# Kernel optimization log

Measured on AMD Instinct MI355X. Metric: run time of the kernel, lower is better.

The kernel has to match this reference:

```python
import jax, jax.numpy as jnp
import numpy as np

B, A, C, H, W = 4, 5, 64, 128, 128


def _base_grid(h, w):
    # torch F.affine_grid with align_corners=False: pixel-center normalized coords
    xs = (2.0 * jnp.arange(w, dtype=jnp.float32) + 1.0) / w - 1.0
    ys = (2.0 * jnp.arange(h, dtype=jnp.float32) + 1.0) / h - 1.0
    X, Y = jnp.meshgrid(xs, ys)  # [h,w]
    return jnp.stack([X, Y, jnp.ones_like(X)], axis=-1)  # [h,w,3]


def _grid_sample(img, grid):
    # img [C,H,W]; grid [H,W,2] = (x,y) normalized; bilinear, zeros padding, align_corners=False
    c, h, w = img.shape
    ix = ((grid[..., 0] + 1.0) * w - 1.0) * 0.5
    iy = ((grid[..., 1] + 1.0) * h - 1.0) * 0.5
    ix0 = jnp.floor(ix); iy0 = jnp.floor(iy)
    ix1 = ix0 + 1.0; iy1 = iy0 + 1.0
    wx1 = ix - ix0; wy1 = iy - iy0
    wx0 = 1.0 - wx1; wy0 = 1.0 - wy1

    def gather(iyf, ixf):
        valid = (iyf >= 0) & (iyf <= h - 1) & (ixf >= 0) & (ixf <= w - 1)
        iyc = jnp.clip(iyf.astype(jnp.int32), 0, h - 1)
        ixc = jnp.clip(ixf.astype(jnp.int32), 0, w - 1)
        return img[:, iyc, ixc] * valid[None].astype(img.dtype)  # [C,H,W]

    return (gather(iy0, ix0) * (wy0 * wx0)[None]
            + gather(iy0, ix1) * (wy0 * wx1)[None]
            + gather(iy1, ix0) * (wy1 * wx0)[None]
            + gather(iy1, ix1) * (wy1 * wx1)[None])


_sample_batch = jax.vmap(_grid_sample)


def setup_inputs() -> dict:
    key = jax.random.key(0)
    k1, k2, k3 = jax.random.split(key, 3)
    feats = jax.random.normal(k1, (B, A, C, H, W), dtype=jnp.float32)
    trans_matrices = jax.random.normal(k2, (B, A, A, 4, 4), dtype=jnp.float32)
    num_agent_tensor = jax.random.randint(k3, (B, A), 1, A + 1, dtype=jnp.int64)
    return {"feats": feats, "trans_matrices": trans_matrices,
            "num_agent_tensor": num_agent_tensor}


def reference(feats, trans_matrices, num_agent_tensor):
    b, a, c, h, w = feats.shape
    T = trans_matrices  # [B,A(target i),A(neighbor j),4,4]
    zeros = jnp.zeros(T.shape[:3], T.dtype)
    ones = jnp.ones_like(zeros)
    # theta_rot = [[T00, T01, 0], [T10, T11, 0]]
    theta_rot = jnp.stack([
        jnp.stack([T[..., 0, 0], T[..., 0, 1], zeros], axis=-1),
        jnp.stack([T[..., 1, 0], T[..., 1, 1], zeros], axis=-1)], axis=-2)
    x_t = 4.0 * T[..., 0, 3] / 128.0
    y_t = -(4.0 * T[..., 1, 3]) / 128.0
    theta_trans = jnp.stack([
        jnp.stack([ones, zeros, x_t], axis=-1),
        jnp.stack([zeros, ones, y_t], axis=-1)], axis=-2)
    base = _base_grid(h, w)  # [H,W,3]
    grid_rot = jnp.einsum('hwk,bijrk->bijhwr', base, theta_rot)
    grid_trans = jnp.einsum('hwk,bijrk->bijhwr', base, theta_trans)
    n = b * a * a
    # neighbor feature feats[b, j] broadcast over target index i
    feats_nb = jnp.broadcast_to(feats[:, None], (b, a, a, c, h, w)).reshape(n, c, h, w)
    w1 = _sample_batch(feats_nb, grid_rot.reshape(n, h, w, 2))
    w2 = _sample_batch(w1, grid_trans.reshape(n, h, w, 2)).reshape(b, a, a, c, h, w)
    na = num_agent_tensor[:, 0]  # [B]
    ar = jnp.arange(a)
    valid = ((ar[None, :, None] < na[:, None, None])
             & (ar[None, None, :] < na[:, None, None])
             & (ar[:, None] != ar[None, :])[None])  # [B,A_i,A_j]
    fused = feats + jnp.sum(w2 * valid[..., None, None, None].astype(feats.dtype), axis=2)
    # agents2batch: concatenate per-agent slices along batch dim -> [A*B, C, H, W]
    return fused.transpose(1, 0, 2, 3, 4).reshape(a * b, c, h, w)
```

## Files before the change

### kernel.cpp

```cpp
#include <hip/hip_runtime.h>


constexpr int Bc = 4, Ac = 5, Cc = 64, Hc = 128, Wc = 128;
constexpr int HWc = Hc * Wc;
constexpr int NP  = Bc * Ac;
constexpr int NG  = Cc / 4;
constexpr int TW = 64, TH = 4;
constexpr int WW = TW + 1, WH = TH + 1, WSZ = WW * WH;
constexpr size_t WS_NEED = (size_t)NP * Cc * HWc * sizeof(float);

__global__ __launch_bounds__(256)
void fafmimo_repack(const float* __restrict__ feats, float4* __restrict__ ws)
{
    const int idx  = (int)(blockIdx.x * 256 + threadIdx.x);
    const int pix4 = (idx & 4095) * 4;
    const int t    = idx >> 12;
    const int g    = t & 15;
    const int p    = t >> 4;
    const float* s = feats + ((size_t)p * Cc + g * 4) * HWc + pix4;
    const float4 r0 = *(const float4*)(s);
    const float4 r1 = *(const float4*)(s + HWc);
    const float4 r2 = *(const float4*)(s + 2 * HWc);
    const float4 r3 = *(const float4*)(s + 3 * HWc);
    float4* d = ws + ((size_t)p * NG + g) * HWc + pix4;
    d[0] = make_float4(r0.x, r1.x, r2.x, r3.x);
    d[1] = make_float4(r0.y, r1.y, r2.y, r3.y);
    d[2] = make_float4(r0.z, r1.z, r2.z, r3.z);
    d[3] = make_float4(r0.w, r1.w, r2.w, r3.w);
}

__global__ __launch_bounds__(256)
void fafmimo_main(const float4* __restrict__ ws,
                  const float* __restrict__ trans,
                  const int*   __restrict__ num_agent,
                  float*       __restrict__ out)
{
    __shared__ float4 w1s[WSZ];

    const int z  = (int)blockIdx.z;
    const int bi = z % NP;
    const int g  = z / NP;
    const int b  = bi / Ac;
    const int i  = bi - b * Ac;
    const int tx = (int)threadIdx.x, ty = (int)threadIdx.y;
    const int tid = ty * TW + tx;
    const int x0 = (int)blockIdx.x * TW, y0 = (int)blockIdx.y * TH;
    const int x  = x0 + tx, y = y0 + ty;
    const int pix = y * Wc + x;
    const int na = num_agent[b * Ac];

    const float xv  = (2.0f * (float)x  + 1.0f) / 128.0f - 1.0f;
    const float yv  = (2.0f * (float)y  + 1.0f) / 128.0f - 1.0f;
    const float xv0 = (2.0f * (float)x0 + 1.0f) / 128.0f - 1.0f;
    const float yv0 = (2.0f * (float)y0 + 1.0f) / 128.0f - 1.0f;

    float4 acc = ws[((size_t)bi * NG + g) * HWc + pix];

    if (i < na) {
        for (int j = 0; j < Ac; ++j) {
            if (j == i || j >= na) continue;

            const float* Tm = trans + (size_t)((b * Ac + i) * Ac + j) * 16;
            const float r00 = Tm[0], r01 = Tm[1], t03 = Tm[3];
            const float r10 = Tm[4], r11 = Tm[5], t13 = Tm[7];
            const float x_t =  (4.0f * t03) / 128.0f;
            const float y_t = -(4.0f * t13) / 128.0f;

            const int fdx = (int)floorf(((xv0 + x_t + 1.0f) * 128.0f - 1.0f) * 0.5f) - x0;
            const int fdy = (int)floorf(((yv0 + y_t + 1.0f) * 128.0f - 1.0f) * 0.5f) - y0;

            const float4* __restrict__ pj =
                ws + ((size_t)((b * Ac + j) * NG) + g) * HWc;

            for (int e = tid; e < WSZ; e += TW * TH) {
                const int ry = e / WW, rx = e - ry * WW;
                const int jy = y0 + fdy + ry, jx = x0 + fdx + rx;
                const int jyc = min(max(jy, 0), 127);
                const int jxc = min(max(jx, 0), 127);

                const float Xs = (2.0f * (float)jxc + 1.0f) / 128.0f - 1.0f;
                const float Ys = (2.0f * (float)jyc + 1.0f) / 128.0f - 1.0f;
                const float gx = Xs * r00 + Ys * r01;
                const float gy = Xs * r10 + Ys * r11;
                const float ixs = ((gx + 1.0f) * 128.0f - 1.0f) * 0.5f;
                const float iys = ((gy + 1.0f) * 128.0f - 1.0f) * 0.5f;
                const float sx0 = floorf(ixs), sy0 = floorf(iys);
                const float u1 = ixs - sx0, v1 = iys - sy0;
                const float u0 = 1.0f - u1, v0 = 1.0f - v1;

                const bool xin = (sx0 >= 0.0f) & (sx0 <= 126.0f);
                const float a  = xin ? u0 : ((sx0 == -1.0f)  ? u1 : 0.0f);
                const float bb = xin ? u1 : ((sx0 == 127.0f) ? u0 : 0.0f);
                const int xb = min(max((int)sx0, 0), 126);

                const bool vr0 = (sy0 >= 0.0f) & (sy0 <= 127.0f);
                const bool vr1 = (sy0 >= -1.0f) & (sy0 <= 126.0f);
                const float wr0 = v0 * (vr0 ? 1.0f : 0.0f);
                const float wr1 = v1 * (vr1 ? 1.0f : 0.0f);
                const int o0 = min(max((int)sy0, 0), 127) * Wc + xb;
                const int o1 = min(max((int)sy0 + 1, 0), 127) * Wc + xb;

                const float4 t0a = pj[o0], t0b = pj[o0 + 1];
                const float4 t1a = pj[o1], t1b = pj[o1 + 1];
                float4 w1;
                w1.x = wr0 * fmaf(a, t0a.x, bb * t0b.x) + wr1 * fmaf(a, t1a.x, bb * t1b.x);
                w1.y = wr0 * fmaf(a, t0a.y, bb * t0b.y) + wr1 * fmaf(a, t1a.y, bb * t1b.y);
                w1.z = wr0 * fmaf(a, t0a.z, bb * t0b.z) + wr1 * fmaf(a, t1a.z, bb * t1b.z);
                w1.w = wr0 * fmaf(a, t0a.w, bb * t0b.w) + wr1 * fmaf(a, t1a.w, bb * t1b.w);
                w1s[e] = w1;
            }
            __syncthreads();

            const float ix2 = ((xv + x_t + 1.0f) * 128.0f - 1.0f) * 0.5f;
            const float iy2 = ((yv + y_t + 1.0f) * 128.0f - 1.0f) * 0.5f;
            const int jx0 = x + fdx, jy0 = y + fdy;
            const float fx1 = ix2 - (float)jx0, fx0 = 1.0f - fx1;
            const float fy1 = iy2 - (float)jy0, fy0 = 1.0f - fy1;
            const float vx0 = (jx0 >= 0 && jx0 <= 127) ? 1.0f : 0.0f;
            const float vx1 = (jx0 >= -1 && jx0 <= 126) ? 1.0f : 0.0f;
            const float vy0 = (jy0 >= 0 && jy0 <= 127) ? 1.0f : 0.0f;
            const float vy1 = (jy0 >= -1 && jy0 <= 126) ? 1.0f : 0.0f;
            const float w00 = fy0 * vy0 * fx0 * vx0;
            const float w01 = fy0 * vy0 * fx1 * vx1;
            const float w10 = fy1 * vy1 * fx0 * vx0;
            const float w11 = fy1 * vy1 * fx1 * vx1;

            const int base = ty * WW + tx;
            const float4 s00 = w1s[base],      s01 = w1s[base + 1];
            const float4 s10 = w1s[base + WW], s11 = w1s[base + WW + 1];
            acc.x += w00 * s00.x + w01 * s01.x + w10 * s10.x + w11 * s11.x;
            acc.y += w00 * s00.y + w01 * s01.y + w10 * s10.y + w11 * s11.y;
            acc.z += w00 * s00.z + w01 * s01.z + w10 * s10.z + w11 * s11.z;
            acc.w += w00 * s00.w + w01 * s01.w + w10 * s10.w + w11 * s11.w;
            __syncthreads();
        }
    }

    float* __restrict__ ob =
        out + ((size_t)(i * Bc + b) * Cc + g * 4) * HWc + pix;
    __builtin_nontemporal_store(acc.x, ob);
    __builtin_nontemporal_store(acc.y, ob + HWc);
    __builtin_nontemporal_store(acc.z, ob + 2 * HWc);
    __builtin_nontemporal_store(acc.w, ob + 3 * HWc);
}

constexpr int CHK = 16;
__global__ __launch_bounds__(256)
void fafmimo_direct(const float* __restrict__ feats,
                    const float* __restrict__ trans,
                    const int*   __restrict__ num_agent,
                    float*       __restrict__ out)
{
    const int z  = (int)blockIdx.z;
    const int bi = z % NP;
    const int c0 = (z / NP) * CHK;
    const int b  = bi / Ac;
    const int i  = bi - b * Ac;
    const int x  = (int)(blockIdx.x * 64 + threadIdx.x);
    const int y  = (int)(blockIdx.y * 4  + threadIdx.y);
    const int pix = y * Wc + x;
    const int na = num_agent[b * Ac];

    const float xv = (2.0f * (float)x + 1.0f) / 128.0f - 1.0f;
    const float yv = (2.0f * (float)y + 1.0f) / 128.0f - 1.0f;

    const float* __restrict__ fi =
        feats + (size_t)(b * Ac + i) * Cc * HWc + (size_t)c0 * HWc;
    float* __restrict__ ob =
        out + (size_t)(i * Bc + b) * Cc * HWc + (size_t)c0 * HWc;

    float acc[CHK];
    #pragma unroll
    for (int k = 0; k < CHK; ++k) acc[k] = fi[k * HWc + pix];

    if (i < na) {
        for (int j = 0; j < Ac; ++j) {
            if (j == i || j >= na) continue;
            const float* Tm = trans + (size_t)((b * Ac + i) * Ac + j) * 16;
            const float r00 = Tm[0], r01 = Tm[1], t03 = Tm[3];
            const float r10 = Tm[4], r11 = Tm[5], t13 = Tm[7];
            const float x_t =  (4.0f * t03) / 128.0f;
            const float y_t = -(4.0f * t13) / 128.0f;
            const float ix2 = ((xv + x_t + 1.0f) * 128.0f - 1.0f) * 0.5f;
            const float iy2 = ((yv + y_t + 1.0f) * 128.0f - 1.0f) * 0.5f;
            const float fx0 = floorf(ix2), fy0 = floorf(iy2);
            const float wx1 = ix2 - fx0,   wy1 = iy2 - fy0;
            const float wx0 = 1.0f - wx1,  wy0 = 1.0f - wy1;

            int off[8]; float wA[8], wB[8];
            #pragma unroll
            for (int cy = 0; cy < 2; ++cy) {
                #pragma unroll
                for (int cx = 0; cx < 2; ++cx) {
                    const float jyf = fy0 + (float)cy;
                    const float jxf = fx0 + (float)cx;
                    const bool v2 = (jyf >= 0.0f) & (jyf <= 127.0f)
                                  & (jxf >= 0.0f) & (jxf <= 127.0f);
                    const float w2 = (cy ? wy1 : wy0) * (cx ? wx1 : wx0)
                                   * (v2 ? 1.0f : 0.0f);
                    const int jy = min(max((int)jyf, 0), 127);
                    const int jx = min(max((int)jxf, 0), 127);
                    const float Xs = (2.0f * (float)jx + 1.0f) / 128.0f - 1.0f;
                    const float Ys = (2.0f * (float)jy + 1.0f) / 128.0f - 1.0f;
                    const float gx = Xs * r00 + Ys * r01;
                    const float gy = Xs * r10 + Ys * r11;
                    const float ixs = ((gx + 1.0f) * 128.0f - 1.0f) * 0.5f;
                    const float iys = ((gy + 1.0f) * 128.0f - 1.0f) * 0.5f;
                    const float sx0 = floorf(ixs), sy0 = floorf(iys);
                    const float u1 = ixs - sx0, v1 = iys - sy0;
                    const float u0 = 1.0f - u1,  v0f = 1.0f - v1;
                    const bool xin = (sx0 >= 0.0f) & (sx0 <= 126.0f);
                    const float a  = xin ? u0 : ((sx0 == -1.0f)  ? u1 : 0.0f);
                    const float bbp = xin ? u1 : ((sx0 == 127.0f) ? u0 : 0.0f);
                    const int xb = min(max((int)sx0, 0), 126);
                    const int e = (cy * 2 + cx) * 2;
                    #pragma unroll
                    for (int r = 0; r < 2; ++r) {
                        const float syr = sy0 + (float)r;
                        const bool vy = (syr >= 0.0f) & (syr <= 127.0f);
                        const float wyr = (r ? v1 : v0f) * (vy ? 1.0f : 0.0f) * w2;
                        const int syc = min(max((int)syr, 0), 127);
                        off[e + r] = syc * Wc + xb;
                        wA[e + r]  = wyr * a;
                        wB[e + r]  = wyr * bbp;
                    }
                }
            }

            const float* __restrict__ fj =
                feats + (size_t)(b * Ac + j) * Cc * HWc + (size_t)c0 * HWc;
            #pragma unroll 4
            for (int k = 0; k < CHK; ++k) {
                const float* __restrict__ p = fj + (size_t)k * HWc;
                float s0 = 0.0f, s1 = 0.0f;
                #pragma unroll
                for (int r = 0; r < 8; ++r) {
                    s0 = fmaf(wA[r], p[off[r]],     s0);
                    s1 = fmaf(wB[r], p[off[r] + 1], s1);
                }
                acc[k] += s0 + s1;
            }
        }
    }

    #pragma unroll
    for (int k = 0; k < CHK; ++k)
        __builtin_nontemporal_store(acc[k], &ob[k * HWc + pix]);
}

extern "C" void kernel_launch(void* const* d_in, const int* in_sizes, int n_in,
                              void* d_out, int out_size, void* d_ws, size_t ws_size,
                              hipStream_t stream) {
    const float* feats     = (const float*)d_in[0];
    const float* trans     = (const float*)d_in[1];
    const int*   num_agent = (const int*)d_in[2];
    float* out = (float*)d_out;

    if (ws_size >= WS_NEED) {
        float4* ws = (float4*)d_ws;
        hipLaunchKernelGGL(fafmimo_repack, dim3(NP * NG * (HWc / 4) / 256),
                           dim3(256), 0, stream, feats, ws);
        dim3 grid(Wc / TW, Hc / TH, NP * NG);
        dim3 block(TW, TH, 1);
        hipLaunchKernelGGL(fafmimo_main, grid, block, 0, stream,
                           ws, trans, num_agent, out);
    } else {
        dim3 grid(Wc / 64, Hc / 4, NP * 4);
        dim3 block(64, 4, 1);
        hipLaunchKernelGGL(fafmimo_direct, grid, block, 0, stream,
                           feats, trans, num_agent, out);
    }
}
```

Measured before the change: 211.1 us.

## Process four channel groups per block to amortize first-stage coordinate math

Each block of the main kernel now handles four float4 channel groups instead of one. The rotation-sample coordinates, weights and clamped offsets are computed once per window element and reused across the four groups. The second-stage weights are likewise reused, and the grid shrinks by a factor of four. The repack kernel also switches to nontemporal vector loads. The cost is four times the shared memory per block, more registers for four accumulators, and fewer blocks in flight.

```diff
diff --git a/kernel.cpp b/kernel.cpp
--- a/kernel.cpp
+++ b/kernel.cpp
@@ -1,12 +1,15 @@
 #include <hip/hip_runtime.h>
 
+
+typedef float floatv4 __attribute__((ext_vector_type(4)));
 
 constexpr int Bc = 4, Ac = 5, Cc = 64, Hc = 128, Wc = 128;
 constexpr int HWc = Hc * Wc;
 constexpr int NP  = Bc * Ac;
 constexpr int NG  = Cc / 4;
+constexpr int GPB = 4;
 constexpr int TW = 64, TH = 4;
-constexpr int WW = TW + 1, WH = TH + 1, WSZ = WW * WH;
+constexpr int WW = TW + 1, WSZ = WW * (TH + 1);
 constexpr size_t WS_NEED = (size_t)NP * Cc * HWc * sizeof(float);
 
 __global__ __launch_bounds__(256)
@@ -17,11 +20,12 @@
     const int t    = idx >> 12;
     const int g    = t & 15;
     const int p    = t >> 4;
-    const float* s = feats + ((size_t)p * Cc + g * 4) * HWc + pix4;
-    const float4 r0 = *(const float4*)(s);
-    const float4 r1 = *(const float4*)(s + HWc);
-    const float4 r2 = *(const float4*)(s + 2 * HWc);
-    const float4 r3 = *(const float4*)(s + 3 * HWc);
+    const floatv4* s =
+        (const floatv4*)(feats + ((size_t)p * Cc + g * 4) * HWc + pix4);
+    const floatv4 r0 = __builtin_nontemporal_load(s);
+    const floatv4 r1 = __builtin_nontemporal_load(s + HWc / 4);
+    const floatv4 r2 = __builtin_nontemporal_load(s + 2 * (HWc / 4));
+    const floatv4 r3 = __builtin_nontemporal_load(s + 3 * (HWc / 4));
     float4* d = ws + ((size_t)p * NG + g) * HWc + pix4;
     d[0] = make_float4(r0.x, r1.x, r2.x, r3.x);
     d[1] = make_float4(r0.y, r1.y, r2.y, r3.y);
@@ -35,11 +39,12 @@
                   const int*   __restrict__ num_agent,
                   float*       __restrict__ out)
 {
-    __shared__ float4 w1s[WSZ];
+    __shared__ float4 w1s[GPB][WSZ];
 
     const int z  = (int)blockIdx.z;
     const int bi = z % NP;
-    const int g  = z / NP;
+    const int q  = z / NP;
+    const int g0 = q * GPB;
     const int b  = bi / Ac;
     const int i  = bi - b * Ac;
     const int tx = (int)threadIdx.x, ty = (int)threadIdx.y;
@@ -54,7 +59,10 @@
     const float xv0 = (2.0f * (float)x0 + 1.0f) / 128.0f - 1.0f;
     const float yv0 = (2.0f * (float)y0 + 1.0f) / 128.0f - 1.0f;
 
-    float4 acc = ws[((size_t)bi * NG + g) * HWc + pix];
+    float4 acc[GPB];
+    #pragma unroll
+    for (int cg = 0; cg < GPB; ++cg)
+        acc[cg] = ws[((size_t)bi * NG + g0 + cg) * HWc + pix];
 
     if (i < na) {
         for (int j = 0; j < Ac; ++j) {
@@ -69,8 +77,10 @@
             const int fdx = (int)floorf(((xv0 + x_t + 1.0f) * 128.0f - 1.0f) * 0.5f) - x0;
             const int fdy = (int)floorf(((yv0 + y_t + 1.0f) * 128.0f - 1.0f) * 0.5f) - y0;
 
-            const float4* __restrict__ pj =
-                ws + ((size_t)((b * Ac + j) * NG) + g) * HWc;
+            const float4* __restrict__ pj0 = ws + ((size_t)((b * Ac + j) * NG) + g0) * HWc;
+            const float4* __restrict__ pj1 = pj0 + HWc;
+            const float4* __restrict__ pj2 = pj0 + 2 * HWc;
+            const float4* __restrict__ pj3 = pj0 + 3 * HWc;
 
             for (int e = tid; e < WSZ; e += TW * TH) {
                 const int ry = e / WW, rx = e - ry * WW;
@@ -100,14 +110,19 @@
                 const int o0 = min(max((int)sy0, 0), 127) * Wc + xb;
                 const int o1 = min(max((int)sy0 + 1, 0), 127) * Wc + xb;
 
-                const float4 t0a = pj[o0], t0b = pj[o0 + 1];
-                const float4 t1a = pj[o1], t1b = pj[o1 + 1];
-                float4 w1;
-                w1.x = wr0 * fmaf(a, t0a.x, bb * t0b.x) + wr1 * fmaf(a, t1a.x, bb * t1b.x);
-                w1.y = wr0 * fmaf(a, t0a.y, bb * t0b.y) + wr1 * fmaf(a, t1a.y, bb * t1b.y);
-                w1.z = wr0 * fmaf(a, t0a.z, bb * t0b.z) + wr1 * fmaf(a, t1a.z, bb * t1b.z);
-                w1.w = wr0 * fmaf(a, t0a.w, bb * t0b.w) + wr1 * fmaf(a, t1a.w, bb * t1b.w);
-                w1s[e] = w1;
+                #pragma unroll
+                for (int cg = 0; cg < GPB; ++cg) {
+                    const float4* __restrict__ pg =
+                        (cg == 0) ? pj0 : (cg == 1) ? pj1 : (cg == 2) ? pj2 : pj3;
+                    const float4 t0a = pg[o0], t0b = pg[o0 + 1];
+                    const float4 t1a = pg[o1], t1b = pg[o1 + 1];
+                    float4 w1;
+                    w1.x = wr0 * fmaf(a, t0a.x, bb * t0b.x) + wr1 * fmaf(a, t1a.x, bb * t1b.x);
+                    w1.y = wr0 * fmaf(a, t0a.y, bb * t0b.y) + wr1 * fmaf(a, t1a.y, bb * t1b.y);
+                    w1.z = wr0 * fmaf(a, t0a.z, bb * t0b.z) + wr1 * fmaf(a, t1a.z, bb * t1b.z);
+                    w1.w = wr0 * fmaf(a, t0a.w, bb * t0b.w) + wr1 * fmaf(a, t1a.w, bb * t1b.w);
+                    w1s[cg][e] = w1;
+                }
             }
             __syncthreads();
 
@@ -126,22 +141,28 @@
             const float w11 = fy1 * vy1 * fx1 * vx1;
 
             const int base = ty * WW + tx;
-            const float4 s00 = w1s[base],      s01 = w1s[base + 1];
-            const float4 s10 = w1s[base + WW], s11 = w1s[base + WW + 1];
-            acc.x += w00 * s00.x + w01 * s01.x + w10 * s10.x + w11 * s11.x;
-            acc.y += w00 * s00.y + w01 * s01.y + w10 * s10.y + w11 * s11.y;
-            acc.z += w00 * s00.z + w01 * s01.z + w10 * s10.z + w11 * s11.z;
-            acc.w += w00 * s00.w + w01 * s01.w + w10 * s10.w + w11 * s11.w;
+            #pragma unroll
+            for (int cg = 0; cg < GPB; ++cg) {
+                const float4 s00 = w1s[cg][base],      s01 = w1s[cg][base + 1];
+                const float4 s10 = w1s[cg][base + WW], s11 = w1s[cg][base + WW + 1];
+                acc[cg].x += w00 * s00.x + w01 * s01.x + w10 * s10.x + w11 * s11.x;
+                acc[cg].y += w00 * s00.y + w01 * s01.y + w10 * s10.y + w11 * s11.y;
+                acc[cg].z += w00 * s00.z + w01 * s01.z + w10 * s10.z + w11 * s11.z;
+                acc[cg].w += w00 * s00.w + w01 * s01.w + w10 * s10.w + w11 * s11.w;
+            }
             __syncthreads();
         }
     }
 
-    float* __restrict__ ob =
-        out + ((size_t)(i * Bc + b) * Cc + g * 4) * HWc + pix;
-    __builtin_nontemporal_store(acc.x, ob);
-    __builtin_nontemporal_store(acc.y, ob + HWc);
-    __builtin_nontemporal_store(acc.z, ob + 2 * HWc);
-    __builtin_nontemporal_store(acc.w, ob + 3 * HWc);
+    #pragma unroll
+    for (int cg = 0; cg < GPB; ++cg) {
+        float* __restrict__ ob =
+            out + ((size_t)(i * Bc + b) * Cc + (g0 + cg) * 4) * HWc + pix;
+        __builtin_nontemporal_store(acc[cg].x, ob);
+        __builtin_nontemporal_store(acc[cg].y, ob + HWc);
+        __builtin_nontemporal_store(acc[cg].z, ob + 2 * HWc);
+        __builtin_nontemporal_store(acc[cg].w, ob + 3 * HWc);
+    }
 }
 
 constexpr int CHK = 16;
@@ -260,7 +281,7 @@
         float4* ws = (float4*)d_ws;
         hipLaunchKernelGGL(fafmimo_repack, dim3(NP * NG * (HWc / 4) / 256),
                            dim3(256), 0, stream, feats, ws);
-        dim3 grid(Wc / TW, Hc / TH, NP * NG);
+        dim3 grid(Wc / TW, Hc / TH, NP * (NG / GPB));
         dim3 block(TW, TH, 1);
         hipLaunchKernelGGL(fafmimo_main, grid, block, 0, stream,
                            ws, trans, num_agent, out);
```

New measurement: 226.2 us. 7.2% more time.
